# Optimization experiments

Hardware: AMD Instinct MI355X
Metric: run time of the kernel (lower is better)

The kernel has to match this reference:

```python
import jax, jax.numpy as jnp
import numpy as np

KSZ = 5   # local window size per spatial dim
NH = 4    # num_channels -> attention heads
EPS = 1e-6

def rmsnorm(x, w):
    return x * jax.lax.rsqrt(jnp.mean(x * x, axis=-1, keepdims=True) + EPS) * w

def local_windows(x, ksz):
    # x: [B, D, H, W, C] -> [B, D, H, W, ksz**3, C] zero-padded SAME windows
    B, D, H, Wd, C = x.shape
    xt = jnp.transpose(x, (0, 4, 1, 2, 3))  # NCDHW
    p = jax.lax.conv_general_dilated_patches(xt, (ksz, ksz, ksz), (1, 1, 1), 'SAME')
    p = p.reshape(B, C, ksz ** 3, D, H, Wd)  # channel-major patch layout
    return jnp.transpose(p, (0, 3, 4, 5, 2, 1))

def forward(x, norm1_w, attn_norm_w, norm2_w, wq, wk, wv, wo, gate_w, up_w, down_w):
    B, D, H, Wd, C = x.shape
    hd = C // NH
    k3 = KSZ ** 3
    h = rmsnorm(x, norm1_w)
    q = (h @ wq).reshape(B, D, H, Wd, NH, hd)
    k = h @ wk
    v = h @ wv
    kwin = local_windows(k, KSZ).reshape(B, D, H, Wd, k3, NH, hd)
    vwin = local_windows(v, KSZ).reshape(B, D, H, Wd, k3, NH, hd)
    scores = jnp.einsum('bxyzhe,bxyzkhe->bxyzhk', q, kwin) / jnp.sqrt(jnp.float32(hd))
    ones = jnp.ones((1, D, H, Wd, 1), x.dtype)
    valid = local_windows(ones, KSZ)[..., 0] > 0.5  # [1,D,H,W,k3] padding mask
    scores = jnp.where(valid[:, :, :, :, None, :], scores, jnp.float32(-1e9))
    attn = jax.nn.softmax(scores, axis=-1)
    o = jnp.einsum('bxyzhk,bxyzkhe->bxyzhe', attn, vwin).reshape(B, D, H, Wd, C)
    x = x + rmsnorm(o @ wo, attn_norm_w)
    h2 = rmsnorm(x, norm2_w)
    x = x + (jax.nn.silu(h2 @ gate_w) * (h2 @ up_w)) @ down_w  # SwiGLU (dropout=eval)
    return x

def setup_inputs():
    key = jax.random.key(0)
    ks = jax.random.split(key, 8)
    width, hidden = 128, 512
    s = 0.02
    return {
        'x': jax.random.normal(ks[0], (1, 16, 16, 16, width), jnp.float32),
        'norm1_w': jnp.ones((width,), jnp.float32),
        'attn_norm_w': jnp.ones((width,), jnp.float32),
        'norm2_w': jnp.ones((width,), jnp.float32),
        'wq': jax.random.normal(ks[1], (width, width), jnp.float32) * s,
        'wk': jax.random.normal(ks[2], (width, width), jnp.float32) * s,
        'wv': jax.random.normal(ks[3], (width, width), jnp.float32) * s,
        'wo': jax.random.normal(ks[4], (width, width), jnp.float32) * s,
        'gate_w': jax.random.normal(ks[5], (width, hidden), jnp.float32) * s,
        'up_w': jax.random.normal(ks[6], (width, hidden), jnp.float32) * s,
        'down_w': jax.random.normal(ks[7], (hidden, width), jnp.float32) * s,
    }

def reference(x, norm1_w, attn_norm_w, norm2_w, wq, wk, wv, wo, gate_w, up_w, down_w):
    return forward(x, norm1_w, attn_norm_w, norm2_w, wq, wk, wv, wo, gate_w, up_w, down_w)
```

## Files before the change

### kernel.cpp

```cpp
#include <hip/hip_runtime.h>
#include <hip/hip_bf16.h>

#define NVOX 4096
#define C    128
#define HID  512
#define EPSF 1e-6f

typedef __attribute__((ext_vector_type(8))) short bf16x8;
typedef __attribute__((ext_vector_type(4))) float f32x4;

__device__ __forceinline__ short f2bs(float f) {
    __hip_bfloat16 h = __float2bfloat16(f);
    short s; __builtin_memcpy(&s, &h, 2); return s;
}
__device__ __forceinline__ float bs2f(unsigned short u) {
    return __uint_as_float(((unsigned)u) << 16);
}

__device__ __forceinline__ bf16x8 lda(const short* hs, int lane, int ks) {
    int r = lane & 15, g = lane >> 4;
    int col = (ks * 32 + g * 8) ^ ((r & 7) << 3);
    return *(const bf16x8*)(hs + r * 128 + col);
}

__device__ __forceinline__ float wave_rsum(float s) {
    s += __shfl_xor(s, 32); s += __shfl_xor(s, 16); s += __shfl_xor(s, 8);
    s += __shfl_xor(s, 4);  s += __shfl_xor(s, 2);  s += __shfl_xor(s, 1);
    return s;
}

__global__ __launch_bounds__(512) void k_prep(
    const float* __restrict__ wq, const float* __restrict__ wk,
    const float* __restrict__ wv, short* __restrict__ wsw)
{
    int id = blockIdx.x * 512 + threadIdx.x;
    int m = id >> 11, loc = id & 2047;
    const float* src = (m == 0) ? wq : (m == 1) ? wk : wv;
    int base = m << 14;
    int ct = loc >> 8, ks = (loc >> 6) & 3, lane = loc & 63;
    int k0 = ks * 32 + (lane >> 4) * 8;
    int c  = ct * 16 + (lane & 15);
    bf16x8 v;
    #pragma unroll
    for (int j = 0; j < 8; j++) v[j] = f2bs(src[(size_t)(k0 + j) * 128 + c]);
    *(bf16x8*)(wsw + base + (((ct * 4 + ks) * 64 + lane) << 3)) = v;
}

__global__ __launch_bounds__(256) void k_qkv(
    const float* __restrict__ x, const float* __restrict__ n1,
    const float* __restrict__ wo, const float* __restrict__ gw,
    const float* __restrict__ uw, const float* __restrict__ dw,
    short* __restrict__ wsw,
    short* __restrict__ qbf, short* __restrict__ kbf, short* __restrict__ vbf)
{
    __shared__ short hs[2048];
    const int r0 = blockIdx.x * 16, t = threadIdx.x;
    const int w = t >> 6, lane = t & 63;

    if (t < 104) {
        int gid = 6144 + blockIdx.x * 104 + t;
        const float* src; int base, ct, ks2, ln2, N, KS;
        if (gid < 8192)       { int loc = gid & 2047;  src = wo; base = 3 << 14; N = 128; KS = 4;
                                ct = loc >> 8; ks2 = (loc >> 6) & 3; ln2 = loc & 63; }
        else if (gid < 16384) { int loc = gid - 8192;  src = gw; base = 65536;  N = 512; KS = 4;
                                ct = loc >> 8; ks2 = (loc >> 6) & 3; ln2 = loc & 63; }
        else if (gid < 24576) { int loc = gid - 16384; src = uw; base = 131072; N = 512; KS = 4;
                                ct = loc >> 8; ks2 = (loc >> 6) & 3; ln2 = loc & 63; }
        else                  { int loc = gid - 24576; src = dw; base = 196608; N = 128; KS = 16;
                                ct = loc >> 10; ks2 = (loc >> 6) & 15; ln2 = loc & 63; }
        int k0 = ks2 * 32 + (ln2 >> 4) * 8;
        int c  = ct * 16 + (ln2 & 15);
        bf16x8 v;
        #pragma unroll
        for (int j = 0; j < 8; j++) v[j] = f2bs(src[(size_t)(k0 + j) * N + c]);
        *(bf16x8*)(wsw + base + (((ct * KS + ks2) * 64 + ln2) << 3)) = v;
    }

    #pragma unroll
    for (int i = 0; i < 4; i++) {
        int r = w * 4 + i;
        const float* xp = x + (size_t)(r0 + r) * 128;
        float v0 = xp[lane], v1 = xp[lane + 64];
        float s = wave_rsum(fmaf(v0, v0, v1 * v1));
        float sc = rsqrtf(s * (1.0f / 128.0f) + EPSF);
        int p3 = (r & 7) << 3;
        hs[r * 128 + (lane ^ p3)]        = f2bs(v0 * sc * n1[lane]);
        hs[r * 128 + ((lane + 64) ^ p3)] = f2bs(v1 * sc * n1[lane + 64]);
    }
    __syncthreads();

    bf16x8 af[4];
    #pragma unroll
    for (int ks = 0; ks < 4; ks++) af[ks] = lda(hs, lane, ks);

    const int rb = (lane >> 4) * 4, cl = lane & 15;
    #pragma unroll
    for (int m = 0; m < 3; m++) {
        const short* wb = wsw + (m << 14);
        f32x4 a0 = {0.f,0.f,0.f,0.f}, a1 = {0.f,0.f,0.f,0.f};
        #pragma unroll
        for (int ks = 0; ks < 4; ks++) {
            bf16x8 b0 = *(const bf16x8*)(wb + ((((w * 2) * 4 + ks) * 64 + lane) << 3));
            bf16x8 b1 = *(const bf16x8*)(wb + ((((w * 2 + 1) * 4 + ks) * 64 + lane) << 3));
            a0 = __builtin_amdgcn_mfma_f32_16x16x32_bf16(af[ks], b0, a0, 0, 0, 0);
            a1 = __builtin_amdgcn_mfma_f32_16x16x32_bf16(af[ks], b1, a1, 0, 0, 0);
        }
        short* outp = (m == 0) ? qbf : (m == 1) ? kbf : vbf;
        short* hp = outp + (size_t)w * NVOX * 32;
        #pragma unroll
        for (int i = 0; i < 4; i++) {
            hp[(size_t)(r0 + rb + i) * 32 + cl]      = f2bs(a0[i]);
            hp[(size_t)(r0 + rb + i) * 32 + 16 + cl] = f2bs(a1[i]);
        }
    }
}

__global__ __launch_bounds__(256) void k_attn(
    const short* __restrict__ qbf, const short* __restrict__ kbf,
    const short* __restrict__ vbf, short* __restrict__ obf)
{
    __shared__ __align__(16) char smem[64128];
    short* K_lds = (short*)smem;
    short* PA    = (short*)smem;
    short* S2    = (short*)(smem + 30720);
    short* VB    = (short*)(smem + 30720);
    short* Q_lds = (short*)(smem + 61440);
    float* inv   = (float*)(smem + 64000);

    const int b = blockIdx.x, head = blockIdx.y, t = threadIdx.x;
    const int ow = (b & 3) * 4, oh = ((b >> 2) & 3) * 4, od = (b >> 4) * 2;
    const int w = t >> 6, lane = t & 63;
    const int g = lane >> 4, r = lane & 15;
    const short* kh = kbf + (size_t)head * NVOX * 32;
    const short* vh = vbf + (size_t)head * NVOX * 32;
    const short* qh = qbf + (size_t)head * NVOX * 32;
    short* oh_ = obf + (size_t)head * NVOX * 32;

    uint4 v0[4] = {}, v1[4] = {};
    {
        int row = t;
        int lw = row & 7, lh = (row >> 3) & 7, ld = row >> 6;
        int gd = od - 2 + ld, gh = oh - 2 + lh, gw_ = ow - 2 + lw;
        int sv = (((unsigned)gd < 16u) && ((unsigned)gh < 16u) && ((unsigned)gw_ < 16u));
        size_t off = (size_t)((((gd << 4) | gh) << 4) | gw_) * 32;
        uint4 kc[4];
        #pragma unroll
        for (int c2 = 0; c2 < 4; c2++) {
            kc[c2] = sv ? *(const uint4*)(kh + off + c2 * 8) : (uint4){0,0,0,0};
            v0[c2] = sv ? *(const uint4*)(vh + off + c2 * 8) : (uint4){0,0,0,0};
        }
        #pragma unroll
        for (int c2 = 0; c2 < 4; c2++) *(uint4*)&K_lds[row * 40 + c2 * 8] = kc[c2];

        if (t >= 128) {
            int row1 = t + 128;
            int lw1 = row1 & 7, lh1 = (row1 >> 3) & 7, ld1 = row1 >> 6;
            int gd1 = od - 2 + ld1, gh1 = oh - 2 + lh1, gw1 = ow - 2 + lw1;
            int sv1 = (((unsigned)gd1 < 16u) && ((unsigned)gh1 < 16u) && ((unsigned)gw1 < 16u));
            size_t off1 = (size_t)((((gd1 << 4) | gh1) << 4) | gw1) * 32;
            uint4 kd[4];
            #pragma unroll
            for (int c2 = 0; c2 < 4; c2++) {
                kd[c2] = sv1 ? *(const uint4*)(kh + off1 + c2 * 8) : (uint4){0,0,0,0};
                v1[c2] = sv1 ? *(const uint4*)(vh + off1 + c2 * 8) : (uint4){0,0,0,0};
            }
            #pragma unroll
            for (int c2 = 0; c2 < 4; c2++) *(uint4*)&K_lds[row1 * 40 + c2 * 8] = kd[c2];
        } else {
            int q = t >> 2, c2q = t & 3;
            int gq = ((od + (q >> 4)) << 8) | ((oh + ((q >> 2) & 3)) << 4) | (ow + (q & 3));
            *(uint4*)&Q_lds[q * 40 + c2q * 8] = *(const uint4*)(qh + (size_t)gq * 32 + c2q * 8);
        }
    }
    __syncthreads();

    {
        bf16x8 bq0 = *(const bf16x8*)(Q_lds + r * 40 + g * 8);
        bf16x8 bq1 = *(const bf16x8*)(Q_lds + (16 + r) * 40 + g * 8);
        #pragma unroll
        for (int jj = 0; jj < 6; jj++) {
            int mt = w + jj * 4;
            bf16x8 ak = *(const bf16x8*)(K_lds + (mt * 16 + r) * 40 + g * 8);
            f32x4 a0 = {0.f,0.f,0.f,0.f}, a1 = {0.f,0.f,0.f,0.f};
            a0 = __builtin_amdgcn_mfma_f32_16x16x32_bf16(ak, bq0, a0, 0, 0, 0);
            a1 = __builtin_amdgcn_mfma_f32_16x16x32_bf16(ak, bq1, a1, 0, 0, 0);
            int key0 = mt * 16 + g * 4;
            short s4[4];
            #pragma unroll
            for (int i = 0; i < 4; i++) s4[i] = f2bs(a0[i]);
            unsigned long long pk0; __builtin_memcpy(&pk0, s4, 8);
            *(unsigned long long*)&S2[r * 392 + key0] = pk0;
            #pragma unroll
            for (int i = 0; i < 4; i++) s4[i] = f2bs(a1[i]);
            unsigned long long pk1; __builtin_memcpy(&pk1, s4, 8);
            *(unsigned long long*)&S2[(16 + r) * 392 + key0] = pk1;
        }
    }
    __syncthreads();

    {
        const int q = t >> 3, kl = t & 7;
        const int qw_ = q & 3, qh_ = (q >> 2) & 3, qd_ = q >> 4;
        const float isq = 0.17677669529663687f;
        uint4 sraw[6];
        #pragma unroll
        for (int jj = 0; jj < 6; jj++)
            sraw[jj] = *(const uint4*)&S2[q * 392 + kl * 48 + jj * 8];
        unsigned long long okb = 0;
        float mx = -1e30f;
        #pragma unroll
        for (int jj = 0; jj < 6; jj++) {
            const unsigned short* u = (const unsigned short*)&sraw[jj];
            #pragma unroll
            for (int e = 0; e < 8; e++) {
                int k = kl * 48 + jj * 8 + e;
                int lw = k & 7, lh = (k >> 3) & 7, ld = k >> 6;
                int ok = ((unsigned)(ld - qd_) <= 4u) & ((unsigned)(lh - qh_) <= 4u)
                       & ((unsigned)(lw - qw_) <= 4u)
                       & ((unsigned)(od - 2 + ld) < 16u) & ((unsigned)(oh - 2 + lh) < 16u)
                       & ((unsigned)(ow - 2 + lw) < 16u);
                float s = bs2f(u[e]) * isq;
                mx = ok ? fmaxf(mx, s) : mx;
                okb |= ((unsigned long long)ok) << (jj * 8 + e);
            }
        }
        mx = fmaxf(mx, __shfl_xor(mx, 1));
        mx = fmaxf(mx, __shfl_xor(mx, 2));
        mx = fmaxf(mx, __shfl_xor(mx, 4));
        float ssum = 0.f;
        #pragma unroll
        for (int jj = 0; jj < 6; jj++) {
            const unsigned short* u = (const unsigned short*)&sraw[jj];
            #pragma unroll
            for (int e = 0; e < 8; e++) {
                int k = kl * 48 + jj * 8 + e;
                float s = bs2f(u[e]) * isq;
                float p = ((okb >> (jj * 8 + e)) & 1) ? __expf(s - mx) : 0.f;
                ssum += p;
                PA[((q >> 4) * 12 + (k >> 5)) * 512 + ((k >> 3) & 3) * 128 + (q & 15) * 8 + (k & 7)] = f2bs(p);
            }
        }
        ssum += __shfl_xor(ssum, 1);
        ssum += __shfl_xor(ssum, 2);
        ssum += __shfl_xor(ssum, 4);
        if (kl == 0) inv[q] = 1.0f / ssum;
    }
    __syncthreads();

    {
        int row = t;
        int ks = row >> 5, g3 = (row >> 3) & 3, j3 = row & 7;
        const unsigned short* u = (const unsigned short*)v0;
        #pragma unroll
        for (int c = 0; c < 32; c++)
            VB[((c >> 4) * 12 + ks) * 512 + g3 * 128 + (c & 15) * 8 + j3] = (short)u[c];
        if (t >= 128) {
            int row1 = t + 128;
            int ks1 = row1 >> 5, g31 = (row1 >> 3) & 3, j31 = row1 & 7;
            const unsigned short* u1 = (const unsigned short*)v1;
            #pragma unroll
            for (int c = 0; c < 32; c++)
                VB[((c >> 4) * 12 + ks1) * 512 + g31 * 128 + (c & 15) * 8 + j31] = (short)u1[c];
        }
    }
    __syncthreads();

    {
        const int mt2 = w >> 1, ct = w & 1;
        f32x4 acc = {0.f,0.f,0.f,0.f};
        #pragma unroll
        for (int ks = 0; ks < 12; ks++) {
            bf16x8 pa = *(const bf16x8*)(PA + (((mt2 * 12 + ks) * 64 + lane) << 3));
            bf16x8 vb = *(const bf16x8*)(VB + (((ct * 12 + ks) * 64 + lane) << 3));
            acc = __builtin_amdgcn_mfma_f32_16x16x32_bf16(pa, vb, acc, 0, 0, 0);
        }
        #pragma unroll
        for (int i = 0; i < 4; i++) {
            int q = mt2 * 16 + g * 4 + i;
            int c = ct * 16 + r;
            int gvox = ((od + (q >> 4)) << 8) | ((oh + ((q >> 2) & 3)) << 4) | (ow + (q & 3));
            oh_[(size_t)gvox * 32 + c] = f2bs(acc[i] * inv[q]);
        }
    }
}

__global__ __launch_bounds__(256) void k_post(
    const short* __restrict__ obf, const short* __restrict__ wsw,
    const float* __restrict__ anw, const float* __restrict__ x,
    const float* __restrict__ n2w, float* __restrict__ out)
{
    __shared__ float ybuf[16][132];
    __shared__ float xres[16][128];
    __shared__ short hs[2048];
    __shared__ short gu[16 * 512];

    const int r0 = blockIdx.x * 16, t = threadIdx.x;
    const int w = t >> 6, lane = t & 63;
    const int ar = lane & 15, ag_ = lane >> 4;

    {
        const short* wb = wsw + (3 << 14);
        f32x4 a0 = {0.f,0.f,0.f,0.f}, a1 = {0.f,0.f,0.f,0.f};
        #pragma unroll
        for (int ks = 0; ks < 4; ks++) {
            bf16x8 a = *(const bf16x8*)(obf + (size_t)ks * NVOX * 32 + (size_t)(r0 + ar) * 32 + ag_ * 8);
            bf16x8 b0 = *(const bf16x8*)(wb + ((((w * 2) * 4 + ks) * 64 + lane) << 3));
            bf16x8 b1 = *(const bf16x8*)(wb + ((((w * 2 + 1) * 4 + ks) * 64 + lane) << 3));
            a0 = __builtin_amdgcn_mfma_f32_16x16x32_bf16(a, b0, a0, 0, 0, 0);
            a1 = __builtin_amdgcn_mfma_f32_16x16x32_bf16(a, b1, a1, 0, 0, 0);
        }
        #pragma unroll
        for (int i = 0; i < 4; i++) {
            ybuf[ag_ * 4 + i][w * 32 + ar]      = a0[i];
            ybuf[ag_ * 4 + i][w * 32 + 16 + ar] = a1[i];
        }
    }
    __syncthreads();

    #pragma unroll
    for (int i = 0; i < 4; i++) {
        int r = w * 4 + i;
        float y0 = ybuf[r][lane], y1 = ybuf[r][lane + 64];
        float s = wave_rsum(fmaf(y0, y0, y1 * y1));
        float sc = rsqrtf(s * (1.0f / 128.0f) + EPSF);
        const float* xp = x + (size_t)(r0 + r) * 128;
        float xr0 = xp[lane]      + y0 * sc * anw[lane];
        float xr1 = xp[lane + 64] + y1 * sc * anw[lane + 64];
        xres[r][lane] = xr0; xres[r][lane + 64] = xr1;
        float s2 = wave_rsum(fmaf(xr0, xr0, xr1 * xr1));
        float sc2 = rsqrtf(s2 * (1.0f / 128.0f) + EPSF);
        int p3 = (r & 7) << 3;
        hs[r * 128 + (lane ^ p3)]        = f2bs(xr0 * sc2 * n2w[lane]);
        hs[r * 128 + ((lane + 64) ^ p3)] = f2bs(xr1 * sc2 * n2w[lane + 64]);
    }
    __syncthreads();

    {
        const short* gwb = wsw + 65536;
        const short* uwb = wsw + 131072;
        bf16x8 af[4];
        #pragma unroll
        for (int ks = 0; ks < 4; ks++) af[ks] = lda(hs, lane, ks);
        f32x4 ag[8], au[8];
        #pragma unroll
        for (int i = 0; i < 8; i++) { ag[i] = (f32x4){0.f,0.f,0.f,0.f}; au[i] = (f32x4){0.f,0.f,0.f,0.f}; }
        #pragma unroll
        for (int ks = 0; ks < 4; ks++) {
            #pragma unroll
            for (int i = 0; i < 8; i++) {
                int ct = w * 8 + i;
                bf16x8 bg = *(const bf16x8*)(gwb + (((ct * 4 + ks) * 64 + lane) << 3));
                bf16x8 bu = *(const bf16x8*)(uwb + (((ct * 4 + ks) * 64 + lane) << 3));
                ag[i] = __builtin_amdgcn_mfma_f32_16x16x32_bf16(af[ks], bg, ag[i], 0, 0, 0);
                au[i] = __builtin_amdgcn_mfma_f32_16x16x32_bf16(af[ks], bu, au[i], 0, 0, 0);
            }
        }
        #pragma unroll
        for (int i = 0; i < 8; i++) {
            int col = (w * 8 + i) * 16 + ar;
            #pragma unroll
            for (int j = 0; j < 4; j++) {
                int row = ag_ * 4 + j;
                float g = ag[i][j], uu = au[i][j];
                float sg = g / (1.0f + __expf(-g));
                gu[row * 512 + (col ^ ((row & 7) << 3))] = f2bs(sg * uu);
            }
        }
    }
    __syncthreads();

    {
        const short* db = wsw + 196608;
        f32x4 a0 = {0.f,0.f,0.f,0.f}, a1 = {0.f,0.f,0.f,0.f};
        #pragma unroll
        for (int ks = 0; ks < 16; ks++) {
            int col = (ks * 32 + ag_ * 8) ^ ((ar & 7) << 3);
            bf16x8 a = *(const bf16x8*)(gu + ar * 512 + col);
            bf16x8 b0 = *(const bf16x8*)(db + ((((w * 2) * 16 + ks) * 64 + lane) << 3));
            bf16x8 b1 = *(const bf16x8*)(db + ((((w * 2 + 1) * 16 + ks) * 64 + lane) << 3));
            a0 = __builtin_amdgcn_mfma_f32_16x16x32_bf16(a, b0, a0, 0, 0, 0);
            a1 = __builtin_amdgcn_mfma_f32_16x16x32_bf16(a, b1, a1, 0, 0, 0);
        }
        #pragma unroll
        for (int i = 0; i < 4; i++) {
            int row = ag_ * 4 + i;
            size_t i0 = (size_t)(r0 + row) * 128 + w * 32 + ar;
            out[i0]      = xres[row][w * 32 + ar]      + a0[i];
            out[i0 + 16] = xres[row][w * 32 + 16 + ar] + a1[i];
        }
    }
}

extern "C" void kernel_launch(void* const* d_in, const int* in_sizes, int n_in,
                              void* d_out, int out_size, void* d_ws, size_t ws_size,
                              hipStream_t stream)
{
    const float* x   = (const float*)d_in[0];
    const float* n1  = (const float*)d_in[1];
    const float* anw = (const float*)d_in[2];
    const float* n2  = (const float*)d_in[3];
    const float* wq  = (const float*)d_in[4];
    const float* wk  = (const float*)d_in[5];
    const float* wv  = (const float*)d_in[6];
    const float* wo  = (const float*)d_in[7];
    const float* gw  = (const float*)d_in[8];
    const float* uw  = (const float*)d_in[9];
    const float* dw  = (const float*)d_in[10];
    float* out = (float*)d_out;

    float* ws = (float*)d_ws;
    short* qbf = (short*)ws;
    short* kbf = (short*)(ws + 262144);
    short* vbf = (short*)(ws + 524288);
    short* obf = (short*)(ws + 786432);
    short* wsw = (short*)(ws + 1048576);

    k_prep<<<12,  512, 0, stream>>>(wq, wk, wv, wsw);
    k_qkv <<<256, 256, 0, stream>>>(x, n1, wo, gw, uw, dw, wsw, qbf, kbf, vbf);
    dim3 ga(128, 4);
    k_attn<<<ga,  256, 0, stream>>>(qbf, kbf, vbf, obf);
    k_post<<<256, 256, 0, stream>>>(obf, wsw, anw, x, n2, out);
}
```

Baseline: 36.74 us.

## Drop prep kernel by converting QKV weights inline; widen qkv/post blocks to 512

Removes the separate k_prep launch. k_qkv now reads wq/wk/wv in fp32 straight from global memory and converts them to bf16 fragments inside each block, so the QKV weights are re-read and re-converted by all 256 blocks. Both k_qkv and k_post now run 512 threads (8 waves), each wave covering one 16-column tile instead of two. This trades one launch and some per-wave register pressure for redundant strided global weight loads.

```diff
diff --git a/kernel.cpp b/kernel.cpp
--- a/kernel.cpp
+++ b/kernel.cpp
@@ -29,25 +29,10 @@
     return s;
 }
 
-__global__ __launch_bounds__(512) void k_prep(
+__global__ __launch_bounds__(512) void k_qkv(
+    const float* __restrict__ x, const float* __restrict__ n1,
     const float* __restrict__ wq, const float* __restrict__ wk,
-    const float* __restrict__ wv, short* __restrict__ wsw)
-{
-    int id = blockIdx.x * 512 + threadIdx.x;
-    int m = id >> 11, loc = id & 2047;
-    const float* src = (m == 0) ? wq : (m == 1) ? wk : wv;
-    int base = m << 14;
-    int ct = loc >> 8, ks = (loc >> 6) & 3, lane = loc & 63;
-    int k0 = ks * 32 + (lane >> 4) * 8;
-    int c  = ct * 16 + (lane & 15);
-    bf16x8 v;
-    #pragma unroll
-    for (int j = 0; j < 8; j++) v[j] = f2bs(src[(size_t)(k0 + j) * 128 + c]);
-    *(bf16x8*)(wsw + base + (((ct * 4 + ks) * 64 + lane) << 3)) = v;
-}
-
-__global__ __launch_bounds__(256) void k_qkv(
-    const float* __restrict__ x, const float* __restrict__ n1,
+    const float* __restrict__ wv,
     const float* __restrict__ wo, const float* __restrict__ gw,
     const float* __restrict__ uw, const float* __restrict__ dw,
     short* __restrict__ wsw,
@@ -56,6 +41,7 @@
     __shared__ short hs[2048];
     const int r0 = blockIdx.x * 16, t = threadIdx.x;
     const int w = t >> 6, lane = t & 63;
+    const int g = lane >> 4, r = lane & 15;
 
     if (t < 104) {
         int gid = 6144 + blockIdx.x * 104 + t;
@@ -77,15 +63,15 @@
     }
 
     #pragma unroll
-    for (int i = 0; i < 4; i++) {
-        int r = w * 4 + i;
-        const float* xp = x + (size_t)(r0 + r) * 128;
+    for (int i = 0; i < 2; i++) {
+        int rr = w * 2 + i;
+        const float* xp = x + (size_t)(r0 + rr) * 128;
         float v0 = xp[lane], v1 = xp[lane + 64];
         float s = wave_rsum(fmaf(v0, v0, v1 * v1));
         float sc = rsqrtf(s * (1.0f / 128.0f) + EPSF);
-        int p3 = (r & 7) << 3;
-        hs[r * 128 + (lane ^ p3)]        = f2bs(v0 * sc * n1[lane]);
-        hs[r * 128 + ((lane + 64) ^ p3)] = f2bs(v1 * sc * n1[lane + 64]);
+        int p3 = (rr & 7) << 3;
+        hs[rr * 128 + (lane ^ p3)]        = f2bs(v0 * sc * n1[lane]);
+        hs[rr * 128 + ((lane + 64) ^ p3)] = f2bs(v1 * sc * n1[lane + 64]);
     }
     __syncthreads();
 
@@ -93,25 +79,28 @@
     #pragma unroll
     for (int ks = 0; ks < 4; ks++) af[ks] = lda(hs, lane, ks);
 
-    const int rb = (lane >> 4) * 4, cl = lane & 15;
+    const int rb = g * 4;
     #pragma unroll
-    for (int m = 0; m < 3; m++) {
-        const short* wb = wsw + (m << 14);
-        f32x4 a0 = {0.f,0.f,0.f,0.f}, a1 = {0.f,0.f,0.f,0.f};
+    for (int i = 0; i < 3; i++) {
+        int gt = w * 3 + i;
+        int m = gt >> 3, ct = gt & 7;
+        const float* srcw = (m == 0) ? wq : (m == 1) ? wk : wv;
+        const float* wp = srcw + ct * 16 + r;
+        f32x4 a0 = {0.f,0.f,0.f,0.f};
         #pragma unroll
         for (int ks = 0; ks < 4; ks++) {
-            bf16x8 b0 = *(const bf16x8*)(wb + ((((w * 2) * 4 + ks) * 64 + lane) << 3));
-            bf16x8 b1 = *(const bf16x8*)(wb + ((((w * 2 + 1) * 4 + ks) * 64 + lane) << 3));
+            const float* wpk = wp + (size_t)(ks * 32 + g * 8) * 128;
+            bf16x8 b0;
+            #pragma unroll
+            for (int j = 0; j < 8; j++) b0[j] = f2bs(wpk[(size_t)j * 128]);
             a0 = __builtin_amdgcn_mfma_f32_16x16x32_bf16(af[ks], b0, a0, 0, 0, 0);
-            a1 = __builtin_amdgcn_mfma_f32_16x16x32_bf16(af[ks], b1, a1, 0, 0, 0);
         }
         short* outp = (m == 0) ? qbf : (m == 1) ? kbf : vbf;
-        short* hp = outp + (size_t)w * NVOX * 32;
-        #pragma unroll
-        for (int i = 0; i < 4; i++) {
-            hp[(size_t)(r0 + rb + i) * 32 + cl]      = f2bs(a0[i]);
-            hp[(size_t)(r0 + rb + i) * 32 + 16 + cl] = f2bs(a1[i]);
-        }
+        short* hp = outp + (size_t)(ct >> 1) * NVOX * 32;
+        int col = (ct & 1) * 16 + r;
+        #pragma unroll
+        for (int j = 0; j < 4; j++)
+            hp[(size_t)(r0 + rb + j) * 32 + col] = f2bs(a0[j]);
     }
 }
 
@@ -284,7 +273,7 @@
     }
 }
 
-__global__ __launch_bounds__(256) void k_post(
+__global__ __launch_bounds__(512) void k_post(
     const short* __restrict__ obf, const short* __restrict__ wsw,
     const float* __restrict__ anw, const float* __restrict__ x,
     const float* __restrict__ n2w, float* __restrict__ out)
@@ -300,26 +289,22 @@
 
     {
         const short* wb = wsw + (3 << 14);
-        f32x4 a0 = {0.f,0.f,0.f,0.f}, a1 = {0.f,0.f,0.f,0.f};
+        f32x4 a0 = {0.f,0.f,0.f,0.f};
         #pragma unroll
         for (int ks = 0; ks < 4; ks++) {
             bf16x8 a = *(const bf16x8*)(obf + (size_t)ks * NVOX * 32 + (size_t)(r0 + ar) * 32 + ag_ * 8);
-            bf16x8 b0 = *(const bf16x8*)(wb + ((((w * 2) * 4 + ks) * 64 + lane) << 3));
-            bf16x8 b1 = *(const bf16x8*)(wb + ((((w * 2 + 1) * 4 + ks) * 64 + lane) << 3));
+            bf16x8 b0 = *(const bf16x8*)(wb + (((w * 4 + ks) * 64 + lane) << 3));
             a0 = __builtin_amdgcn_mfma_f32_16x16x32_bf16(a, b0, a0, 0, 0, 0);
-            a1 = __builtin_amdgcn_mfma_f32_16x16x32_bf16(a, b1, a1, 0, 0, 0);
-        }
-        #pragma unroll
-        for (int i = 0; i < 4; i++) {
-            ybuf[ag_ * 4 + i][w * 32 + ar]      = a0[i];
-            ybuf[ag_ * 4 + i][w * 32 + 16 + ar] = a1[i];
-        }
+        }
+        #pragma unroll
+        for (int i = 0; i < 4; i++)
+            ybuf[ag_ * 4 + i][w * 16 + ar] = a0[i];
     }
     __syncthreads();
 
     #pragma unroll
-    for (int i = 0; i < 4; i++) {
-        int r = w * 4 + i;
+    for (int i = 0; i < 2; i++) {
+        int r = w * 2 + i;
         float y0 = ybuf[r][lane], y1 = ybuf[r][lane + 64];
         float s = wave_rsum(fmaf(y0, y0, y1 * y1));
         float sc = rsqrtf(s * (1.0f / 128.0f) + EPSF);
@@ -341,14 +326,14 @@
         bf16x8 af[4];
         #pragma unroll
         for (int ks = 0; ks < 4; ks++) af[ks] = lda(hs, lane, ks);
-        f32x4 ag[8], au[8];
-        #pragma unroll
-        for (int i = 0; i < 8; i++) { ag[i] = (f32x4){0.f,0.f,0.f,0.f}; au[i] = (f32x4){0.f,0.f,0.f,0.f}; }
+        f32x4 ag[4], au[4];
+        #pragma unroll
+        for (int i = 0; i < 4; i++) { ag[i] = (f32x4){0.f,0.f,0.f,0.f}; au[i] = (f32x4){0.f,0.f,0.f,0.f}; }
         #pragma unroll
         for (int ks = 0; ks < 4; ks++) {
             #pragma unroll
-            for (int i = 0; i < 8; i++) {
-                int ct = w * 8 + i;
+            for (int i = 0; i < 4; i++) {
+                int ct = w * 4 + i;
                 bf16x8 bg = *(const bf16x8*)(gwb + (((ct * 4 + ks) * 64 + lane) << 3));
                 bf16x8 bu = *(const bf16x8*)(uwb + (((ct * 4 + ks) * 64 + lane) << 3));
                 ag[i] = __builtin_amdgcn_mfma_f32_16x16x32_bf16(af[ks], bg, ag[i], 0, 0, 0);
@@ -356,8 +341,8 @@
             }
         }
         #pragma unroll
-        for (int i = 0; i < 8; i++) {
-            int col = (w * 8 + i) * 16 + ar;
+        for (int i = 0; i < 4; i++) {
+            int col = (w * 4 + i) * 16 + ar;
             #pragma unroll
             for (int j = 0; j < 4; j++) {
                 int row = ag_ * 4 + j;
@@ -371,22 +356,19 @@
 
     {
         const short* db = wsw + 196608;
-        f32x4 a0 = {0.f,0.f,0.f,0.f}, a1 = {0.f,0.f,0.f,0.f};
+        f32x4 a0 = {0.f,0.f,0.f,0.f};
         #pragma unroll
         for (int ks = 0; ks < 16; ks++) {
             int col = (ks * 32 + ag_ * 8) ^ ((ar & 7) << 3);
             bf16x8 a = *(const bf16x8*)(gu + ar * 512 + col);
-            bf16x8 b0 = *(const bf16x8*)(db + ((((w * 2) * 16 + ks) * 64 + lane) << 3));
-            bf16x8 b1 = *(const bf16x8*)(db + ((((w * 2 + 1) * 16 + ks) * 64 + lane) << 3));
+            bf16x8 b0 = *(const bf16x8*)(db + (((w * 16 + ks) * 64 + lane) << 3));
             a0 = __builtin_amdgcn_mfma_f32_16x16x32_bf16(a, b0, a0, 0, 0, 0);
-            a1 = __builtin_amdgcn_mfma_f32_16x16x32_bf16(a, b1, a1, 0, 0, 0);
         }
         #pragma unroll
         for (int i = 0; i < 4; i++) {
             int row = ag_ * 4 + i;
-            size_t i0 = (size_t)(r0 + row) * 128 + w * 32 + ar;
-            out[i0]      = xres[row][w * 32 + ar]      + a0[i];
-            out[i0 + 16] = xres[row][w * 32 + 16 + ar] + a1[i];
+            size_t i0 = (size_t)(r0 + row) * 128 + w * 16 + ar;
+            out[i0] = xres[row][w * 16 + ar] + a0[i];
         }
     }
 }
@@ -415,9 +397,8 @@
     short* obf = (short*)(ws + 786432);
     short* wsw = (short*)(ws + 1048576);
 
-    k_prep<<<12,  512, 0, stream>>>(wq, wk, wv, wsw);
-    k_qkv <<<256, 256, 0, stream>>>(x, n1, wo, gw, uw, dw, wsw, qbf, kbf, vbf);
+    k_qkv <<<256, 512, 0, stream>>>(x, n1, wq, wk, wv, wo, gw, uw, dw, wsw, qbf, kbf, vbf);
     dim3 ga(128, 4);
     k_attn<<<ga,  256, 0, stream>>>(qbf, kbf, vbf, obf);
-    k_post<<<256, 256, 0, stream>>>(obf, wsw, anw, x, n2, out);
-}
+    k_post<<<256, 512, 0, stream>>>(obf, wsw, anw, x, n2, out);
+}
```

New measurement: 33.50 us. 8.8% less time.
